# Kernel tuning notes

Measured on AMD Instinct MI355X. Metric: run time of the kernel, lower is better.

Reference implementation:

```python
import jax, jax.numpy as jnp
import numpy as np

N_CHARS, EMB, HID, SEQ = 256, 512, 2048, 8192


def setup_inputs() -> dict:
    key = jax.random.key(0)
    ks = jax.random.split(key, 12)
    s = 0.02
    cat = EMB + HID
    return {
        "input_seq": jax.random.randint(ks[0], (SEQ,), 0, N_CHARS, dtype=jnp.int32),
        "hidden": jnp.zeros((HID,), jnp.float32),
        "cell": jnp.zeros((HID,), jnp.float32),
        "embedding": jax.random.normal(ks[1], (N_CHARS, EMB), jnp.float32) * s,
        "Wf": jax.random.normal(ks[2], (HID, cat), jnp.float32) * s,
        "bf": jax.random.normal(ks[3], (HID,), jnp.float32) * s,
        "Wi": jax.random.normal(ks[4], (HID, cat), jnp.float32) * s,
        "bi": jax.random.normal(ks[5], (HID,), jnp.float32) * s,
        "Wo": jax.random.normal(ks[6], (HID, cat), jnp.float32) * s,
        "bo": jax.random.normal(ks[7], (HID,), jnp.float32) * s,
        "Wc": jax.random.normal(ks[8], (HID, cat), jnp.float32) * s,
        "bc": jax.random.normal(ks[9], (HID,), jnp.float32) * s,
        "Wout": jax.random.normal(ks[10], (N_CHARS, HID), jnp.float32) * s,
        "bout": jax.random.normal(ks[11], (N_CHARS,), jnp.float32) * s,
    }


def reference(input_seq, hidden, cell, embedding, Wf, bf, Wi, bi, Wo, bo, Wc, bc, Wout, bout):
    def step(carry, idx):
        h, c = carry
        x = embedding[idx]                       # [EMB]
        z = jnp.concatenate([x, h])              # [EMB+HID], order matches torch concat([i, h])
        f = jax.nn.sigmoid(Wf @ z + bf)
        i = jax.nn.sigmoid(Wi @ z + bi)
        o = jax.nn.sigmoid(Wo @ z + bo)
        c_tilde = jnp.tanh(Wc @ z + bc)
        c_new = f * c + i * c_tilde
        h_new = o * jnp.tanh(c_new)
        pred = Wout @ h_new + bout               # [N_CHARS]
        return (h_new, c_new), pred

    (h, c), outs = jax.lax.scan(step, (hidden, cell), input_seq)
    return outs, h, c  # outs: [SEQ, N_CHARS]
```

## Files before the change

### kernel.cpp

```cpp
#include <hip/hip_runtime.h>
#include <cstdint>
#include <cstddef>

#define SEQ   8192
#define EMB   512
#define HID   2048
#define NCH   256
#define CAT   (EMB + HID)
#define NBLK  256
#define NTH   512
#define NROW  8192

typedef unsigned int u32x4 __attribute__((ext_vector_type(4)));

__device__ __forceinline__ unsigned long long packpair(float v, unsigned tag) {
    return ((unsigned long long)tag << 32) | (unsigned long long)__float_as_uint(v);
}

#define DPP_ADD(x, ctrl) \
    x += __int_as_float(__builtin_amdgcn_update_dpp(0, __float_as_int(x), ctrl, 0xF, 0xF, true))

__device__ __forceinline__ float wave_sum(float x) {
    DPP_ADD(x, 0x111);
    DPP_ADD(x, 0x112);
    DPP_ADD(x, 0x114);
    DPP_ADD(x, 0x118);
    x += __shfl_xor(x, 16, 64);
    x += __shfl_xor(x, 32, 64);
    return x;
}

#define ST4(N0,N1,N2,N3, V) asm volatile( \
    "v_accvgpr_write_b32 a" #N0 ", %0\n\t" \
    "v_accvgpr_write_b32 a" #N1 ", %1\n\t" \
    "v_accvgpr_write_b32 a" #N2 ", %2\n\t" \
    "v_accvgpr_write_b32 a" #N3 ", %3" \
    :: "v"((V).x), "v"((V).y), "v"((V).z), "v"((V).w) \
    : "a" #N0, "a" #N1, "a" #N2, "a" #N3)

#define DOT16(A0,A1,A2,A3, B0,B1,B2,B3, C0,C1,C2,C3, D0,D1,D2,D3, Z0,Z1,Z2,Z3) \
    "v_accvgpr_read_b32 v68, a" #A0 "\n\t" \
    "v_accvgpr_read_b32 v69, a" #B0 "\n\t" \
    "v_accvgpr_read_b32 v70, a" #C0 "\n\t" \
    "v_accvgpr_read_b32 v71, a" #D0 "\n\t" \
    "v_fmac_f32 %0, v68, " Z0 "\n\t" \
    "v_accvgpr_read_b32 v68, a" #A1 "\n\t" \
    "v_fmac_f32 %1, v69, " Z0 "\n\t" \
    "v_accvgpr_read_b32 v69, a" #B1 "\n\t" \
    "v_fmac_f32 %2, v70, " Z0 "\n\t" \
    "v_accvgpr_read_b32 v70, a" #C1 "\n\t" \
    "v_fmac_f32 %3, v71, " Z0 "\n\t" \
    "v_accvgpr_read_b32 v71, a" #D1 "\n\t" \
    "v_fmac_f32 %0, v68, " Z1 "\n\t" \
    "v_accvgpr_read_b32 v68, a" #A2 "\n\t" \
    "v_fmac_f32 %1, v69, " Z1 "\n\t" \
    "v_accvgpr_read_b32 v69, a" #B2 "\n\t" \
    "v_fmac_f32 %2, v70, " Z1 "\n\t" \
    "v_accvgpr_read_b32 v70, a" #C2 "\n\t" \
    "v_fmac_f32 %3, v71, " Z1 "\n\t" \
    "v_accvgpr_read_b32 v71, a" #D2 "\n\t" \
    "v_fmac_f32 %0, v68, " Z2 "\n\t" \
    "v_accvgpr_read_b32 v68, a" #A3 "\n\t" \
    "v_fmac_f32 %1, v69, " Z2 "\n\t" \
    "v_accvgpr_read_b32 v69, a" #B3 "\n\t" \
    "v_fmac_f32 %2, v70, " Z2 "\n\t" \
    "v_accvgpr_read_b32 v70, a" #C3 "\n\t" \
    "v_fmac_f32 %3, v71, " Z2 "\n\t" \
    "v_accvgpr_read_b32 v71, a" #D3 "\n\t" \
    "v_fmac_f32 %0, v68, " Z3 "\n\t" \
    "v_fmac_f32 %1, v69, " Z3 "\n\t" \
    "v_fmac_f32 %2, v70, " Z3 "\n\t" \
    "v_fmac_f32 %3, v71, " Z3 "\n\t"

#define ACLOB \
    "a0","a1","a2","a3","a4","a5","a6","a7","a8","a9", \
    "a10","a11","a12","a13","a14","a15","a16","a17","a18","a19", \
    "a20","a21","a22","a23","a24","a25","a26","a27","a28","a29", \
    "a30","a31","a32","a33","a34","a35","a36","a37","a38","a39", \
    "a40","a41","a42","a43","a44","a45","a46","a47","a48","a49", \
    "a50","a51","a52","a53","a54","a55","a56","a57","a58","a59", \
    "a60","a61","a62","a63","a64","a65","a66","a67","a68","a69", \
    "a70","a71","a72","a73","a74","a75","a76","a77","a78","a79", \
    "a80","a81","a82","a83","a84","a85","a86","a87","a88","a89", \
    "a90","a91","a92","a93","a94","a95","a96","a97","a98","a99", \
    "a100","a101","a102","a103","a104","a105","a106","a107","a108","a109", \
    "a110","a111","a112","a113","a114","a115","a116","a117","a118","a119", \
    "a120","a121","a122","a123","a124","a125","a126","a127"
#define VCLOB \
    "v60","v61","v62","v63","v64","v65","v66","v67","v68","v69","v70","v71"

__global__ __launch_bounds__(256)
void build_ptab(const float* __restrict__ emb,
                const float* __restrict__ Wf, const float* __restrict__ Wi,
                const float* __restrict__ Wo, const float* __restrict__ Wc,
                const float* __restrict__ bfv, const float* __restrict__ biv,
                const float* __restrict__ bov, const float* __restrict__ bcv,
                float* __restrict__ P)
{
    const int r = blockIdx.x;
    const int j = r >> 2, g = r & 3;
    const float* W = (g == 0 ? Wf : g == 1 ? Wi : g == 2 ? Wo : Wc) + (size_t)j * CAT;
    const float  b = (g == 0 ? bfv : g == 1 ? biv : g == 2 ? bov : bcv)[j];
    const float* x = emb + (size_t)threadIdx.x * EMB;
    float acc = 0.f;
    #pragma unroll 8
    for (int k = 0; k < EMB; k += 4) {
        const float4 w4 = *(const float4*)(W + k);
        const float4 x4 = *(const float4*)(x + k);
        acc = fmaf(w4.x, x4.x, acc); acc = fmaf(w4.y, x4.y, acc);
        acc = fmaf(w4.z, x4.z, acc); acc = fmaf(w4.w, x4.w, acc);
    }
    P[((size_t)threadIdx.x << 13) + r] = acc + b;
}

__global__
__attribute__((amdgpu_flat_work_group_size(NTH, NTH)))
__attribute__((amdgpu_waves_per_eu(2, 2)))
void lstm_persistent(const int* __restrict__ seq,
                     const float* __restrict__ h0,
                     const float* __restrict__ c0,
                     const float* __restrict__ Wf, const float* __restrict__ Wi,
                     const float* __restrict__ Wo, const float* __restrict__ Wc,
                     const float* __restrict__ Wout, const float* __restrict__ boutv,
                     const float* __restrict__ Ptab,
                     float* __restrict__ out,
                     unsigned long long* __restrict__ hbuf)
{
    const int cu  = blockIdx.x;
    const int tid = threadIdx.x;
    const int wv  = tid >> 6;
    const int ln  = tid & 63;
    const int j   = cu * 8 + wv;

    __shared__ float z_lds[HID];
    __shared__ float wred[8];
    __shared__ float hpub[8];

    {
        const float* r0 = Wf + (size_t)j * CAT + EMB + 4 * ln;
        const float* r1 = Wi + (size_t)j * CAT + EMB + 4 * ln;
        const float* r2 = Wo + (size_t)j * CAT + EMB + 4 * ln;
        const float* r3 = Wc + (size_t)j * CAT + EMB + 4 * ln;
        float4 v;
        v = *(const float4*)(r0 +    0); ST4(0,1,2,3, v);
        v = *(const float4*)(r0 +  256); ST4(4,5,6,7, v);
        v = *(const float4*)(r0 +  512); ST4(8,9,10,11, v);
        v = *(const float4*)(r0 +  768); ST4(12,13,14,15, v);
        v = *(const float4*)(r0 + 1024); ST4(16,17,18,19, v);
        v = *(const float4*)(r0 + 1280); ST4(20,21,22,23, v);
        v = *(const float4*)(r0 + 1536); ST4(24,25,26,27, v);
        v = *(const float4*)(r0 + 1792); ST4(28,29,30,31, v);
        v = *(const float4*)(r1 +    0); ST4(32,33,34,35, v);
        v = *(const float4*)(r1 +  256); ST4(36,37,38,39, v);
        v = *(const float4*)(r1 +  512); ST4(40,41,42,43, v);
        v = *(const float4*)(r1 +  768); ST4(44,45,46,47, v);
        v = *(const float4*)(r1 + 1024); ST4(48,49,50,51, v);
        v = *(const float4*)(r1 + 1280); ST4(52,53,54,55, v);
        v = *(const float4*)(r1 + 1536); ST4(56,57,58,59, v);
        v = *(const float4*)(r1 + 1792); ST4(60,61,62,63, v);
        v = *(const float4*)(r2 +    0); ST4(64,65,66,67, v);
        v = *(const float4*)(r2 +  256); ST4(68,69,70,71, v);
        v = *(const float4*)(r2 +  512); ST4(72,73,74,75, v);
        v = *(const float4*)(r2 +  768); ST4(76,77,78,79, v);
        v = *(const float4*)(r2 + 1024); ST4(80,81,82,83, v);
        v = *(const float4*)(r2 + 1280); ST4(84,85,86,87, v);
        v = *(const float4*)(r2 + 1536); ST4(88,89,90,91, v);
        v = *(const float4*)(r2 + 1792); ST4(92,93,94,95, v);
        v = *(const float4*)(r3 +    0); ST4(96,97,98,99, v);
        v = *(const float4*)(r3 +  256); ST4(100,101,102,103, v);
        v = *(const float4*)(r3 +  512); ST4(104,105,106,107, v);
        v = *(const float4*)(r3 +  768); ST4(108,109,110,111, v);
        v = *(const float4*)(r3 + 1024); ST4(112,113,114,115, v);
        v = *(const float4*)(r3 + 1280); ST4(116,117,118,119, v);
        v = *(const float4*)(r3 + 1536); ST4(120,121,122,123, v);
        v = *(const float4*)(r3 + 1792); ST4(124,125,126,127, v);
    }
    const float4 ww = *(const float4*)(Wout + (size_t)cu * HID + tid * 4);
    const float bout_cu = boutv[cu];
    const unsigned zaddr = (unsigned)(size_t)&z_lds[4 * ln];

    float c = c0[j];

    if (tid < 8) {
        const int jm = cu * 8 + tid;
        __hip_atomic_store(&hbuf[jm], packpair(h0[jm], 1u),
                           __ATOMIC_RELAXED, __HIP_MEMORY_SCOPE_AGENT);
    }

    int budget = 1 << 22;
    float hv0 = 0.f, hv1 = 0.f, hv2 = 0.f, hv3 = 0.f;
    int ch = seq[0];

    #pragma unroll 1
    for (int t = 0; t < SEQ; ++t) {
        int chv = ch;
        asm volatile("" : "+v"(chv));
        const float4 p4 = *(const float4*)(Ptab + ((size_t)(unsigned)chv << 13) + (j << 2));
        if (t + 1 < SEQ) ch = seq[t + 1];

        {
            const unsigned long long* p = hbuf + (size_t)(t & 1) * HID + tid * 4;
            const unsigned want = (unsigned)(t + 1);
            u32x4 q0, q1;
            while (true) {
                asm volatile(
                    "global_load_dwordx4 %0, %2, off sc0 sc1\n\t"
                    "global_load_dwordx4 %1, %3, off sc0 sc1\n\t"
                    "s_waitcnt vmcnt(0)"
                    : "=&v"(q0), "=&v"(q1)
                    : "v"(p), "v"(p + 2)
                    : "memory");
                if (q0.y == want && q0.w == want && q1.y == want && q1.w == want) break;
                if (--budget < 0) break;
                __builtin_amdgcn_s_sleep(1);
            }
            hv0 = __uint_as_float(q0.x);
            hv1 = __uint_as_float(q0.z);
            hv2 = __uint_as_float(q1.x);
            hv3 = __uint_as_float(q1.z);
        }
        *(float4*)&z_lds[tid * 4] = make_float4(hv0, hv1, hv2, hv3);
        __syncthreads();

        float ac0 = 0.f, ac1 = 0.f, ac2 = 0.f, ac3 = 0.f;
        asm volatile(
            "s_waitcnt lgkmcnt(0)\n\t"
            "ds_read_b128 v[60:63], %[za] offset:0\n\t"
            "ds_read_b128 v[64:67], %[za] offset:1024\n\t"
            "s_waitcnt lgkmcnt(1)\n\t"
            DOT16(0,1,2,3, 32,33,34,35, 64,65,66,67, 96,97,98,99, "v60","v61","v62","v63")
            "ds_read_b128 v[60:63], %[za] offset:2048\n\t"
            "s_waitcnt lgkmcnt(1)\n\t"
            DOT16(4,5,6,7, 36,37,38,39, 68,69,70,71, 100,101,102,103, "v64","v65","v66","v67")
            "ds_read_b128 v[64:67], %[za] offset:3072\n\t"
            "s_waitcnt lgkmcnt(1)\n\t"
            DOT16(8,9,10,11, 40,41,42,43, 72,73,74,75, 104,105,106,107, "v60","v61","v62","v63")
            "ds_read_b128 v[60:63], %[za] offset:4096\n\t"
            "s_waitcnt lgkmcnt(1)\n\t"
            DOT16(12,13,14,15, 44,45,46,47, 76,77,78,79, 108,109,110,111, "v64","v65","v66","v67")
            "ds_read_b128 v[64:67], %[za] offset:5120\n\t"
            "s_waitcnt lgkmcnt(1)\n\t"
            DOT16(16,17,18,19, 48,49,50,51, 80,81,82,83, 112,113,114,115, "v60","v61","v62","v63")
            "ds_read_b128 v[60:63], %[za] offset:6144\n\t"
            "s_waitcnt lgkmcnt(1)\n\t"
            DOT16(20,21,22,23, 52,53,54,55, 84,85,86,87, 116,117,118,119, "v64","v65","v66","v67")
            "ds_read_b128 v[64:67], %[za] offset:7168\n\t"
            "s_waitcnt lgkmcnt(1)\n\t"
            DOT16(24,25,26,27, 56,57,58,59, 88,89,90,91, 120,121,122,123, "v60","v61","v62","v63")
            "s_waitcnt lgkmcnt(0)\n\t"
            DOT16(28,29,30,31, 60,61,62,63, 92,93,94,95, 124,125,126,127, "v64","v65","v66","v67")
            : "+v"(ac0), "+v"(ac1), "+v"(ac2), "+v"(ac3)
            : [za] "v"(zaddr)
            : ACLOB, VCLOB, "memory");

        float aw = fmaf(ww.x, hv0, fmaf(ww.y, hv1, fmaf(ww.z, hv2, ww.w * hv3)));

        ac0 = wave_sum(ac0); ac1 = wave_sum(ac1);
        ac2 = wave_sum(ac2); ac3 = wave_sum(ac3);
        aw  = wave_sum(aw);

        if (ln == 63) {
            const float gf = 1.f / (1.f + __expf(-(ac0 + p4.x)));
            const float gi = 1.f / (1.f + __expf(-(ac1 + p4.y)));
            const float go = 1.f / (1.f + __expf(-(ac2 + p4.z)));
            const float ct = tanhf(ac3 + p4.w);
            c = fmaf(gf, c, gi * ct);
            hpub[wv] = go * tanhf(c);
            wred[wv] = aw;
        }
        __syncthreads();
        if (tid < 8) {
            __hip_atomic_store(&hbuf[(size_t)((t + 1) & 1) * HID + cu * 8 + tid],
                               packpair(hpub[tid], (unsigned)(t + 2)),
                               __ATOMIC_RELAXED, __HIP_MEMORY_SCOPE_AGENT);
        }
        if (tid == NTH - 1 && t >= 1) {
            float s = bout_cu;
            #pragma unroll
            for (int q = 0; q < 8; ++q) s += wred[q];
            out[(size_t)(t - 1) * NCH + cu] = s;
        }
    }

    {
        const unsigned long long* p = hbuf + (size_t)(SEQ & 1) * HID + tid * 4;
        const unsigned want = (unsigned)(SEQ + 1);
        u32x4 q0, q1;
        while (true) {
            asm volatile(
                "global_load_dwordx4 %0, %2, off sc0 sc1\n\t"
                "global_load_dwordx4 %1, %3, off sc0 sc1\n\t"
                "s_waitcnt vmcnt(0)"
                : "=&v"(q0), "=&v"(q1)
                : "v"(p), "v"(p + 2)
                : "memory");
            if (q0.y == want && q0.w == want && q1.y == want && q1.w == want) break;
            if (--budget < 0) break;
            __builtin_amdgcn_s_sleep(1);
        }
        hv0 = __uint_as_float(q0.x);
        hv1 = __uint_as_float(q0.z);
        hv2 = __uint_as_float(q1.x);
        hv3 = __uint_as_float(q1.z);

        float aw = fmaf(ww.x, hv0, fmaf(ww.y, hv1, fmaf(ww.z, hv2, ww.w * hv3)));
        aw = wave_sum(aw);
        if (ln == 63) wred[wv] = aw;
        __syncthreads();
        if (tid == NTH - 1) {
            float s = bout_cu;
            #pragma unroll
            for (int q = 0; q < 8; ++q) s += wred[q];
            out[(size_t)(SEQ - 1) * NCH + cu] = s;
        }
        if (cu == 0) {
            *(float4*)&out[(size_t)SEQ * NCH + tid * 4] =
                make_float4(hv0, hv1, hv2, hv3);
        }
        if (ln == 63) out[(size_t)SEQ * NCH + HID + j] = c;
    }
}

extern "C" void kernel_launch(void* const* d_in, const int* in_sizes, int n_in,
                              void* d_out, int out_size, void* d_ws, size_t ws_size,
                              hipStream_t stream)
{
    const int*   seq  = (const int*)  d_in[0];
    const float* h0   = (const float*)d_in[1];
    const float* c0   = (const float*)d_in[2];
    const float* emb  = (const float*)d_in[3];
    const float* Wf   = (const float*)d_in[4];
    const float* bf_  = (const float*)d_in[5];
    const float* Wi   = (const float*)d_in[6];
    const float* bi_  = (const float*)d_in[7];
    const float* Wo   = (const float*)d_in[8];
    const float* bo_  = (const float*)d_in[9];
    const float* Wc   = (const float*)d_in[10];
    const float* bc_  = (const float*)d_in[11];
    const float* Wout = (const float*)d_in[12];
    const float* bout = (const float*)d_in[13];
    float* out = (float*)d_out;

    unsigned long long* hbuf = (unsigned long long*)d_ws;
    float* Ptab = (float*)((char*)d_ws + 2 * HID * sizeof(unsigned long long));

    build_ptab<<<dim3(NROW), dim3(256), 0, stream>>>(
        emb, Wf, Wi, Wo, Wc, bf_, bi_, bo_, bc_, Ptab);

    void* args[] = { (void*)&seq, (void*)&h0, (void*)&c0,
                     (void*)&Wf, (void*)&Wi, (void*)&Wo, (void*)&Wc,
                     (void*)&Wout, (void*)&bout, (void*)&Ptab,
                     (void*)&out, (void*)&hbuf };

    hipError_t e = hipLaunchCooperativeKernel((void*)lstm_persistent,
                                              dim3(NBLK), dim3(NTH),
                                              args, 0, stream);
    if (e != hipSuccess) {
        lstm_persistent<<<dim3(NBLK), dim3(NTH), 0, stream>>>(
            seq, h0, c0, Wf, Wi, Wo, Wc, Wout, bout, Ptab, out, hbuf);
    }
}
```

Measured before the change: 22.79 ms.

## Replace block barriers with per-wave LDS flags and double-buffered hidden state

Removes both __syncthreads per timestep. Each wave writes its slice of h into a double-buffered LDS array and raises a per-wave flag, and consumers spin only on the flags of the chunks they are about to read, so the dot product on the first half can start before all waves arrive. Each wave publishes its own h element directly to global memory, and the Wout output reduction is deferred by one step through a 4-deep LDS ring that rotates which wave does it. It also swaps the sigmoid and tanh for rcp/exp approximations, which adds LDS spin traffic and depends on the flag ordering being correct.

```diff
diff --git a/kernel.cpp b/kernel.cpp
--- a/kernel.cpp
+++ b/kernel.cpp
@@ -15,6 +15,13 @@
 
 __device__ __forceinline__ unsigned long long packpair(float v, unsigned tag) {
     return ((unsigned long long)tag << 32) | (unsigned long long)__float_as_uint(v);
+}
+
+__device__ __forceinline__ float fast_sig(float x) {
+    return __builtin_amdgcn_rcpf(1.f + __expf(-x));
+}
+__device__ __forceinline__ float fast_tanh(float x) {
+    return 1.f - 2.f * __builtin_amdgcn_rcpf(__expf(2.f * x) + 1.f);
 }
 
 #define DPP_ADD(x, ctrl) \
@@ -132,9 +139,10 @@
     const int ln  = tid & 63;
     const int j   = cu * 8 + wv;
 
-    __shared__ float z_lds[HID];
-    __shared__ float wred[8];
-    __shared__ float hpub[8];
+    __shared__ float z[2][HID];
+    __shared__ int   Fl[2 * 8];
+    __shared__ float wredL[4][8];
+    __shared__ float wfin[8];
 
     {
         const float* r0 = Wf + (size_t)j * CAT + EMB + 4 * ln;
@@ -177,13 +185,14 @@
     }
     const float4 ww = *(const float4*)(Wout + (size_t)cu * HID + tid * 4);
     const float bout_cu = boutv[cu];
-    const unsigned zaddr = (unsigned)(size_t)&z_lds[4 * ln];
 
     float c = c0[j];
 
-    if (tid < 8) {
-        const int jm = cu * 8 + tid;
-        __hip_atomic_store(&hbuf[jm], packpair(h0[jm], 1u),
+    if (tid < 16) Fl[tid] = 0;
+    __syncthreads();
+
+    if (ln == 63) {
+        __hip_atomic_store(&hbuf[j], packpair(h0[j], 1u),
                            __ATOMIC_RELAXED, __HIP_MEMORY_SCOPE_AGENT);
     }
 
@@ -191,16 +200,21 @@
     float hv0 = 0.f, hv1 = 0.f, hv2 = 0.f, hv3 = 0.f;
     int ch = seq[0];
 
+#define SPINF(cc) do { volatile int* fp = &Fl[par * 8 + (cc)]; \
+        while (*fp != want) { if (--budget < 0) break; } } while (0)
+
     #pragma unroll 1
     for (int t = 0; t < SEQ; ++t) {
+        const int par = t & 1;
+        const unsigned want = (unsigned)(t + 1);
+
         int chv = ch;
         asm volatile("" : "+v"(chv));
         const float4 p4 = *(const float4*)(Ptab + ((size_t)(unsigned)chv << 13) + (j << 2));
         if (t + 1 < SEQ) ch = seq[t + 1];
 
         {
-            const unsigned long long* p = hbuf + (size_t)(t & 1) * HID + tid * 4;
-            const unsigned want = (unsigned)(t + 1);
+            const unsigned long long* p = hbuf + (size_t)par * HID + tid * 4;
             u32x4 q0, q1;
             while (true) {
                 asm volatile(
@@ -219,12 +233,16 @@
             hv2 = __uint_as_float(q1.x);
             hv3 = __uint_as_float(q1.z);
         }
-        *(float4*)&z_lds[tid * 4] = make_float4(hv0, hv1, hv2, hv3);
-        __syncthreads();
+
+        *(float4*)&z[par][4 * tid] = make_float4(hv0, hv1, hv2, hv3);
+        asm volatile("s_waitcnt lgkmcnt(0)" ::: "memory");
+        if (ln == 63) *((volatile int*)&Fl[par * 8 + wv]) = (int)want;
+
+        const unsigned za = (unsigned)(size_t)&z[par][4 * ln];
 
         float ac0 = 0.f, ac1 = 0.f, ac2 = 0.f, ac3 = 0.f;
+        SPINF(0); SPINF(1); SPINF(2); SPINF(3);
         asm volatile(
-            "s_waitcnt lgkmcnt(0)\n\t"
             "ds_read_b128 v[60:63], %[za] offset:0\n\t"
             "ds_read_b128 v[64:67], %[za] offset:1024\n\t"
             "s_waitcnt lgkmcnt(1)\n\t"
@@ -235,9 +253,14 @@
             "ds_read_b128 v[64:67], %[za] offset:3072\n\t"
             "s_waitcnt lgkmcnt(1)\n\t"
             DOT16(8,9,10,11, 40,41,42,43, 72,73,74,75, 104,105,106,107, "v60","v61","v62","v63")
+            "s_waitcnt lgkmcnt(0)\n\t"
+            DOT16(12,13,14,15, 44,45,46,47, 76,77,78,79, 108,109,110,111, "v64","v65","v66","v67")
+            : "+v"(ac0), "+v"(ac1), "+v"(ac2), "+v"(ac3)
+            : [za] "v"(za)
+            : ACLOB, VCLOB, "memory");
+        SPINF(4); SPINF(5); SPINF(6); SPINF(7);
+        asm volatile(
             "ds_read_b128 v[60:63], %[za] offset:4096\n\t"
-            "s_waitcnt lgkmcnt(1)\n\t"
-            DOT16(12,13,14,15, 44,45,46,47, 76,77,78,79, 108,109,110,111, "v64","v65","v66","v67")
             "ds_read_b128 v[64:67], %[za] offset:5120\n\t"
             "s_waitcnt lgkmcnt(1)\n\t"
             DOT16(16,17,18,19, 48,49,50,51, 80,81,82,83, 112,113,114,115, "v60","v61","v62","v63")
@@ -250,7 +273,7 @@
             "s_waitcnt lgkmcnt(0)\n\t"
             DOT16(28,29,30,31, 60,61,62,63, 92,93,94,95, 124,125,126,127, "v64","v65","v66","v67")
             : "+v"(ac0), "+v"(ac1), "+v"(ac2), "+v"(ac3)
-            : [za] "v"(zaddr)
+            : [za] "v"(za)
             : ACLOB, VCLOB, "memory");
 
         float aw = fmaf(ww.x, hv0, fmaf(ww.y, hv1, fmaf(ww.z, hv2, ww.w * hv3)));
@@ -260,27 +283,26 @@
         aw  = wave_sum(aw);
 
         if (ln == 63) {
-            const float gf = 1.f / (1.f + __expf(-(ac0 + p4.x)));
-            const float gi = 1.f / (1.f + __expf(-(ac1 + p4.y)));
-            const float go = 1.f / (1.f + __expf(-(ac2 + p4.z)));
-            const float ct = tanhf(ac3 + p4.w);
+            const float gf = fast_sig(ac0 + p4.x);
+            const float gi = fast_sig(ac1 + p4.y);
+            const float go = fast_sig(ac2 + p4.z);
+            const float ct = fast_tanh(ac3 + p4.w);
             c = fmaf(gf, c, gi * ct);
-            hpub[wv] = go * tanhf(c);
-            wred[wv] = aw;
-        }
-        __syncthreads();
-        if (tid < 8) {
-            __hip_atomic_store(&hbuf[(size_t)((t + 1) & 1) * HID + cu * 8 + tid],
-                               packpair(hpub[tid], (unsigned)(t + 2)),
+            const float hn = go * fast_tanh(c);
+            wredL[t & 3][wv] = aw;
+            asm volatile("s_waitcnt lgkmcnt(0)" ::: "memory");
+            __hip_atomic_store(&hbuf[(size_t)((t + 1) & 1) * HID + j],
+                               packpair(hn, (unsigned)(t + 2)),
                                __ATOMIC_RELAXED, __HIP_MEMORY_SCOPE_AGENT);
         }
-        if (tid == NTH - 1 && t >= 1) {
+        if (ln == 62 && wv == (t & 7) && t >= 2) {
             float s = bout_cu;
             #pragma unroll
-            for (int q = 0; q < 8; ++q) s += wred[q];
-            out[(size_t)(t - 1) * NCH + cu] = s;
-        }
-    }
+            for (int q = 0; q < 8; ++q) s += wredL[(t - 1) & 3][q];
+            out[(size_t)(t - 2) * NCH + cu] = s;
+        }
+    }
+#undef SPINF
 
     {
         const unsigned long long* p = hbuf + (size_t)(SEQ & 1) * HID + tid * 4;
@@ -305,13 +327,17 @@
 
         float aw = fmaf(ww.x, hv0, fmaf(ww.y, hv1, fmaf(ww.z, hv2, ww.w * hv3)));
         aw = wave_sum(aw);
-        if (ln == 63) wred[wv] = aw;
+        if (ln == 63) wfin[wv] = aw;
         __syncthreads();
         if (tid == NTH - 1) {
-            float s = bout_cu;
+            float s1 = bout_cu, s2 = bout_cu;
             #pragma unroll
-            for (int q = 0; q < 8; ++q) s += wred[q];
-            out[(size_t)(SEQ - 1) * NCH + cu] = s;
+            for (int q = 0; q < 8; ++q) {
+                s1 += wredL[(SEQ - 1) & 3][q];
+                s2 += wfin[q];
+            }
+            out[(size_t)(SEQ - 2) * NCH + cu] = s1;
+            out[(size_t)(SEQ - 1) * NCH + cu] = s2;
         }
         if (cu == 0) {
             *(float4*)&out[(size_t)SEQ * NCH + tid * 4] =
```

Measured after the change: 56.47 ms. 148% more time.
